# Optimization experiments

Hardware: AMD Instinct MI355X
Metric: run time of the kernel (lower is better)

Reference implementation:

```python
import jax, jax.numpy as jnp
import numpy as np

H = 16        # num_heads
D = 128       # head_dim = hidden_size // num_heads
HID = 2048    # hidden_size
BLOCK = 64    # moba_chunk_size
TOPK = 8      # moba_topk


def setup_inputs() -> dict:
    key = jax.random.key(0)
    ks = jax.random.split(key, 5)
    B, S = 1, 2048
    hidden_states = jax.random.normal(ks[0], (B, S, HID), dtype=jnp.float32)
    scale = HID ** -0.5
    Wq = jax.random.normal(ks[1], (HID, H * D), dtype=jnp.float32) * scale
    Wk = jax.random.normal(ks[2], (HID, H * D), dtype=jnp.float32) * scale
    Wv = jax.random.normal(ks[3], (HID, H * D), dtype=jnp.float32) * scale
    Wo = jax.random.normal(ks[4], (H * D, HID), dtype=jnp.float32) * scale
    return {"hidden_states": hidden_states, "Wq": Wq, "Wk": Wk, "Wv": Wv, "Wo": Wo}


def _moba_forward(hidden_states, Wq, Wk, Wv, Wo):
    B, S, _ = hidden_states.shape
    nb = S // BLOCK
    INF = jnp.float32(jnp.inf)

    q = (hidden_states @ Wq).reshape(B, S, H, D)
    k = (hidden_states @ Wk).reshape(B, S, H, D)
    v = (hidden_states @ Wv).reshape(B, S, H, D)

    # MoBA gating: mean-pooled key per block -> [B, nb, H, D]
    kg = k.reshape(B, nb, BLOCK, H, D).mean(axis=2)
    gate = jnp.einsum('bshd,bnhd->bhsn', q, kg)  # [B,H,S,nb]

    pos = jnp.arange(S)
    qb = pos // BLOCK                 # query's own block
    blk = jnp.arange(nb)
    is_self = qb[:, None] == blk[None, :]                      # self block always selected
    not_past = pos[:, None] < (blk[None, :] + 1) * BLOCK       # blocks not fully in the past
    gate = jnp.where(is_self, INF, jnp.where(not_past, -INF, gate))

    kk = min(TOPK, nb)
    topv, topi = jax.lax.top_k(gate, kk)                       # [B,H,S,kk]
    thresh = topv.min(axis=-1, keepdims=True)
    idx_mask = (topi[..., None] == blk).any(axis=-2)           # [B,H,S,nb]
    need = (gate >= thresh) & idx_mask
    gate_bias = jnp.where(need, 0.0, -INF)                     # additive block mask

    sm_scale = D ** -0.5
    qk = jnp.einsum('bshd,bthd->bhst', q, k) * sm_scale        # [B,H,S,S]
    qk = qk.reshape(B, H, S, nb, BLOCK) + gate_bias[..., None]
    qk = qk.reshape(B, H, S, S)
    causal = pos[:, None] >= pos[None, :]
    qk = jnp.where(causal, qk, -INF)

    p = jax.nn.softmax(qk, axis=-1)
    o = jnp.einsum('bhst,bthd->bshd', p, v).reshape(B, S, H * D)
    return o @ Wo


def reference(hidden_states, Wq, Wk, Wv, Wo):
    # Returns (output, attentions=None, past_key_values=None) in the original;
    # only the output tensor matters for correctness.
    return _moba_forward(hidden_states, Wq, Wk, Wv, Wo)
```

## Files before the change

kernel.cpp:

```cpp
#include <hip/hip_runtime.h>
#include <hip/hip_bf16.h>
#include <stdint.h>
#include <stddef.h>


using bh = __bf16;
typedef __bf16 bhx8 __attribute__((ext_vector_type(8)));
typedef __bf16 bhx4 __attribute__((ext_vector_type(4)));
typedef float  f32x4 __attribute__((ext_vector_type(4)));

#define SEQ   2048
#define HIDN  2048
#define NHEAD 16
#define HDIM  128
#define NBLK  32
#define BLKSZ 64
#define NQKV  6144
#define NGATE 512
#define LDC   136
#define PSTRIDE ((size_t)SEQ * NGATE)

#define GLDS16(gsrc, ldst)                                                     \
  __builtin_amdgcn_global_load_lds(                                            \
      (const __attribute__((address_space(1))) uint32_t*)(gsrc),               \
      (__attribute__((address_space(3))) uint32_t*)(ldst), 16, 0, 0)

__global__ __launch_bounds__(256) void prep(const float* __restrict__ hs,
                                            bh* __restrict__ hs_hi, bh* __restrict__ hs_lo,
                                            const float* __restrict__ Wq, const float* __restrict__ Wk,
                                            const float* __restrict__ Wv, const float* __restrict__ Wo,
                                            bh* __restrict__ wqkvT, bh* __restrict__ woT,
                                            float* __restrict__ hsm) {
  __shared__ float tile[32][33];
  const int b = blockIdx.x;
  const int t = threadIdx.x;
  if (b < 16384) {
    const int z = b >> 12;
    const int x = b & 63, y = (b >> 6) & 63;
    const float* in = (z == 0) ? Wq : (z == 1) ? Wk : (z == 2) ? Wv : Wo;
    bh* out = (z < 3) ? (wqkvT + (size_t)z * HIDN * HIDN) : woT;
    const int tx = t & 31, ty = t >> 5;
    const int c0 = x * 32, r0 = y * 32;
#pragma unroll
    for (int i = 0; i < 4; i++)
      tile[ty + i * 8][tx] = in[(size_t)(r0 + ty + i * 8) * HIDN + c0 + tx];
    __syncthreads();
#pragma unroll
    for (int i = 0; i < 4; i++)
      out[(size_t)(c0 + ty + i * 8) * HIDN + r0 + tx] = (bh)tile[tx][ty + i * 8];
  } else if (b < 16384 + 4096) {
    int i = ((b - 16384) * 256 + t) * 4;
    float4 v = *(const float4*)(hs + i);
    bhx4 h4, l4;
    float vv[4] = {v.x, v.y, v.z, v.w};
#pragma unroll
    for (int e = 0; e < 4; e++) {
      bh h = (bh)vv[e];
      h4[e] = h;
      l4[e] = (bh)(vv[e] - (float)h);
    }
    *(bhx4*)(hs_hi + i) = h4;
    *(bhx4*)(hs_lo + i) = l4;
  } else {
    int idx = (b - 20480) * 256 + t;
    int n = idx >> 11, c = idx & 2047;
    const float* p = hs + (size_t)(n * BLKSZ) * HIDN + c;
    float s = 0.f;
#pragma unroll 8
    for (int r = 0; r < BLKSZ; r++) s += p[(size_t)r * HIDN];
    hsm[idx] = s * (1.0f / 64.0f);
  }
}

#define GEMM_STAGE_TILE(SRC, r0_, ldsbase)                                       \
  {                                                                              \
    _Pragma("unroll")                                                            \
    for (int it_ = 0; it_ < 4; it_++) {                                          \
      int idx_ = it_ * 256 + t;                                                  \
      int row_ = idx_ >> 3, x_ = (idx_ & 7) << 4;                                \
      GLDS16((const char*)(SRC) + (size_t)(r0_ + row_) * strideB + kbyte +       \
                 (x_ ^ ((row_ & 7) << 4)),                                       \
             (char*)(ldsbase) + ((idx_ >> 6) << 10));                            \
    }                                                                            \
  }

__global__ __launch_bounds__(256) void qkvkg(const bh* __restrict__ A, const bh* __restrict__ BT,
                                             bh* __restrict__ Cb,
                                             const float* __restrict__ hsm,
                                             const float* __restrict__ Wk,
                                             float* __restrict__ part) {
  __shared__ __align__(16) char smraw[128 * LDC * 2];
  const int t = threadIdx.x;

  if (blockIdx.x < 768) {
    bh* smem = (bh*)smraw;
    bh* As = smem;
    bh* Bs = smem + 128 * 64;
    const int L = t & 63, w = t >> 6;
    const int wm = w & 1, wn = w >> 1;
    const int quad = L >> 4, lo = L & 15;
    const int m0 = (blockIdx.x / 48) * 128, n0 = (blockIdx.x % 48) * 128;
    const size_t strideB = (size_t)HIDN * 2;

    f32x4 acc[4][4];
#pragma unroll
    for (int i = 0; i < 4; i++)
#pragma unroll
      for (int j = 0; j < 4; j++) acc[i][j] = (f32x4){0.f, 0.f, 0.f, 0.f};

    for (int k0 = 0; k0 < HIDN; k0 += 64) {
      const size_t kbyte = (size_t)k0 * 2;
      GEMM_STAGE_TILE(A, m0, As);
      GEMM_STAGE_TILE(BT, n0, Bs);
      __syncthreads();
#pragma unroll
      for (int ks = 0; ks < 2; ks++) {
        bhx8 af[4], bf_[4];
#pragma unroll
        for (int i = 0; i < 4; i++) {
          const int row = wm * 64 + i * 16 + lo;
          af[i] = *(const bhx8*)((const char*)As + row * 128 +
                                 ((ks * 64 + quad * 16) ^ ((row & 7) << 4)));
        }
#pragma unroll
        for (int j = 0; j < 4; j++) {
          const int row = wn * 64 + j * 16 + lo;
          bf_[j] = *(const bhx8*)((const char*)Bs + row * 128 +
                                  ((ks * 64 + quad * 16) ^ ((row & 7) << 4)));
        }
#pragma unroll
        for (int i = 0; i < 4; i++)
#pragma unroll
          for (int j = 0; j < 4; j++)
            acc[i][j] = __builtin_amdgcn_mfma_f32_16x16x32_bf16(af[i], bf_[j], acc[i][j], 0, 0, 0);
      }
      __syncthreads();
    }

    bh* Cs = smem;
#pragma unroll
    for (int i = 0; i < 4; i++)
#pragma unroll
      for (int j = 0; j < 4; j++)
#pragma unroll
        for (int r = 0; r < 4; r++)
          Cs[(wm * 64 + i * 16 + quad * 4 + r) * LDC + wn * 64 + j * 16 + lo] = (bh)acc[i][j][r];
    __syncthreads();
#pragma unroll
    for (int it = 0; it < 8; it++) {
      int idx = it * 256 + t;
      int row = idx >> 4, cg = idx & 15;
      *(uint4*)(Cb + (size_t)(m0 + row) * NQKV + n0 + cg * 8) = *(const uint4*)&Cs[row * LDC + cg * 8];
    }
  } else {
    float (*hl)[32] = (float (*)[32])smraw;
    const int b2 = blockIdx.x - 768;
    const int c = (b2 & 7) * 256 + t;
    const int ky = b2 >> 3;
    const int k0 = ky * 32;
    for (int i = t; i < 32 * 32; i += 256)
      hl[i >> 5][i & 31] = hsm[(size_t)(i >> 5) * HIDN + k0 + (i & 31)];
    __syncthreads();
    float acc[32];
#pragma unroll
    for (int n = 0; n < 32; n++) acc[n] = 0.f;
#pragma unroll 2
    for (int k4 = 0; k4 < 8; k4++) {
      float w0 = Wk[(size_t)(k0 + k4 * 4 + 0) * HIDN + c];
      float w1 = Wk[(size_t)(k0 + k4 * 4 + 1) * HIDN + c];
      float w2 = Wk[(size_t)(k0 + k4 * 4 + 2) * HIDN + c];
      float w3 = Wk[(size_t)(k0 + k4 * 4 + 3) * HIDN + c];
#pragma unroll
      for (int n = 0; n < 32; n++) {
        float4 hv = *(const float4*)&hl[n][k4 * 4];
        acc[n] += hv.x * w0 + hv.y * w1 + hv.z * w2 + hv.w * w3;
      }
    }
#pragma unroll
    for (int n = 0; n < 32; n++)
      part[((size_t)ky * 32 + n) * HIDN + c] = acc[n];
  }
}

__global__ __launch_bounds__(256) void gemm_bt128f(const bh* __restrict__ A, const bh* __restrict__ BT,
                                                   float* __restrict__ Cf, int M, int N, int K) {
  __shared__ __align__(16) bh smem[2 * 128 * 64];
  bh* As = smem;
  bh* Bs = smem + 128 * 64;
  const int t = threadIdx.x;
  const int L = t & 63, w = t >> 6;
  const int wm = w & 1, wn = w >> 1;
  const int quad = L >> 4, lo = L & 15;
  const int m0 = blockIdx.y * 128, n0 = blockIdx.x * 128;
  const size_t strideB = (size_t)K * 2;

  f32x4 acc[4][4];
#pragma unroll
  for (int i = 0; i < 4; i++)
#pragma unroll
    for (int j = 0; j < 4; j++) acc[i][j] = (f32x4){0.f, 0.f, 0.f, 0.f};

  for (int k0 = 0; k0 < K; k0 += 64) {
    const size_t kbyte = (size_t)k0 * 2;
    GEMM_STAGE_TILE(A, m0, As);
    GEMM_STAGE_TILE(BT, n0, Bs);
    __syncthreads();
#pragma unroll
    for (int ks = 0; ks < 2; ks++) {
      bhx8 af[4], bf_[4];
#pragma unroll
      for (int i = 0; i < 4; i++) {
        const int row = wm * 64 + i * 16 + lo;
        af[i] = *(const bhx8*)((const char*)As + row * 128 +
                               ((ks * 64 + quad * 16) ^ ((row & 7) << 4)));
      }
#pragma unroll
      for (int j = 0; j < 4; j++) {
        const int row = wn * 64 + j * 16 + lo;
        bf_[j] = *(const bhx8*)((const char*)Bs + row * 128 +
                                ((ks * 64 + quad * 16) ^ ((row & 7) << 4)));
      }
#pragma unroll
      for (int i = 0; i < 4; i++)
#pragma unroll
        for (int j = 0; j < 4; j++)
          acc[i][j] = __builtin_amdgcn_mfma_f32_16x16x32_bf16(af[i], bf_[j], acc[i][j], 0, 0, 0);
    }
    __syncthreads();
  }

#pragma unroll
  for (int i = 0; i < 4; i++)
#pragma unroll
    for (int j = 0; j < 4; j++)
#pragma unroll
      for (int r = 0; r < 4; r++) {
        int row = m0 + wm * 64 + i * 16 + quad * 4 + r;
        int col = n0 + wn * 64 + j * 16 + lo;
        Cf[(size_t)row * N + col] = acc[i][j][r];
      }
}

__global__ __launch_bounds__(256) void gemm_gate_split(const bh* __restrict__ hs_hi,
                                                       const bh* __restrict__ hs_lo,
                                                       const bh* __restrict__ wg_hi,
                                                       const bh* __restrict__ wg_lo,
                                                       float* __restrict__ part6,
                                                       float* __restrict__ part2) {
  __shared__ __align__(16) bh smem[2 * 128 * 64];
  bh* As = smem;
  bh* Bs = smem + 128 * 64;
  const int t = threadIdx.x;
  const int L = t & 63, w = t >> 6;
  const int wm = w & 1, wn = w >> 1;
  const int quad = L >> 4, lo = L & 15;
  const int m0 = blockIdx.y * 128, n0 = blockIdx.x * 128;
  const int z = blockIdx.z;
  const size_t strideB = (size_t)HIDN * 2;

  f32x4 acc[4][4];
#pragma unroll
  for (int i = 0; i < 4; i++)
#pragma unroll
    for (int j = 0; j < 4; j++) acc[i][j] = (f32x4){0.f, 0.f, 0.f, 0.f};

  for (int k0 = 0; k0 < 768; k0 += 64) {
    const int vk = z * 768 + k0;
    const int ph = vk >> 11;
    const bh* Ap = (ph == 1) ? hs_lo : hs_hi;
    const bh* Bp = (ph == 2) ? wg_lo : wg_hi;
    const size_t kbyte = (size_t)(vk & 2047) * 2;
    GEMM_STAGE_TILE(Ap, m0, As);
    GEMM_STAGE_TILE(Bp, n0, Bs);
    __syncthreads();
#pragma unroll
    for (int ks = 0; ks < 2; ks++) {
      bhx8 af[4], bf_[4];
#pragma unroll
      for (int i = 0; i < 4; i++) {
        const int row = wm * 64 + i * 16 + lo;
        af[i] = *(const bhx8*)((const char*)As + row * 128 +
                               ((ks * 64 + quad * 16) ^ ((row & 7) << 4)));
      }
#pragma unroll
      for (int j = 0; j < 4; j++) {
        const int row = wn * 64 + j * 16 + lo;
        bf_[j] = *(const bhx8*)((const char*)Bs + row * 128 +
                                ((ks * 64 + quad * 16) ^ ((row & 7) << 4)));
      }
#pragma unroll
      for (int i = 0; i < 4; i++)
#pragma unroll
        for (int j = 0; j < 4; j++)
          acc[i][j] = __builtin_amdgcn_mfma_f32_16x16x32_bf16(af[i], bf_[j], acc[i][j], 0, 0, 0);
    }
    __syncthreads();
  }

  float* outp = (z < 6) ? (part6 + (size_t)z * PSTRIDE) : (part2 + (size_t)(z - 6) * PSTRIDE);
#pragma unroll
  for (int i = 0; i < 4; i++)
#pragma unroll
    for (int j = 0; j < 4; j++)
#pragma unroll
      for (int r = 0; r < 4; r++) {
        int row = m0 + wm * 64 + i * 16 + quad * 4 + r;
        int col = n0 + wn * 64 + j * 16 + lo;
        outp[(size_t)row * NGATE + col] = acc[i][j][r];
      }
}

__global__ __launch_bounds__(256) void kg_reduce64(const float* __restrict__ part, float* __restrict__ kg) {
  int idx = blockIdx.x * 256 + threadIdx.x;
  float s = 0.f;
#pragma unroll
  for (int kc = 0; kc < 64; kc++) s += part[(size_t)kc * 65536 + idx];
  kg[idx] = s;
}

__global__ __launch_bounds__(256) void wgk_vtrans(const float* __restrict__ Wq,
                                                  const float* __restrict__ kg,
                                                  bh* __restrict__ wg_hi, bh* __restrict__ wg_lo,
                                                  const bh* __restrict__ qkv, bh* __restrict__ vt) {
  __shared__ __align__(16) char smraw[49792];
  const int b = blockIdx.x;
  const int t = threadIdx.x;
  if (b < 4096) {
    float (*tile)[33] = (float (*)[33])smraw;
    const int tx = t & 31, ty = t >> 5;
    const int s0 = (b & 63) * 32, d0 = ((b >> 6) & 3) * 32, h = b >> 8;
#pragma unroll
    for (int i = 0; i < 4; i++)
      tile[ty + i * 8][tx] = (float)qkv[(size_t)(s0 + ty + i * 8) * NQKV + 2 * HIDN + h * HDIM + d0 + tx];
    __syncthreads();
#pragma unroll
    for (int i = 0; i < 4; i++)
      vt[((size_t)h * HDIM + d0 + ty + i * 8) * SEQ + s0 + tx] = (bh)tile[tx][ty + i * 8];
  } else {
    float (*wst)[65] = (float (*)[65])smraw;
    float (*kl)[129] = (float (*)[129])(smraw + 33280);
    const int b2 = b - 4096;
    const int h = b2 >> 3;
    const int r0 = (b2 & 7) * 256;
    const int rloc = t & 63, ng = t >> 6;

    for (int i = t; i < 32 * 128; i += 256)
      kl[i >> 7][i & 127] = kg[(size_t)(i >> 7) * HIDN + h * HDIM + (i & 127)];

#pragma unroll
    for (int rt = 0; rt < 4; rt++) {
      __syncthreads();
      for (int i = t; i < 64 * 128; i += 256) {
        int row = i >> 7, col = i & 127;
        wst[col][row] = Wq[(size_t)(r0 + rt * 64 + row) * HIDN + h * HDIM + col];
      }
      __syncthreads();
      float acc8[8];
#pragma unroll
      for (int nn = 0; nn < 8; nn++) acc8[nn] = 0.f;
      for (int d = 0; d < 128; d++) {
        float wv = wst[d][rloc];
#pragma unroll
        for (int nn = 0; nn < 8; nn++)
          acc8[nn] += wv * kl[ng * 8 + nn][d];
      }
#pragma unroll
      for (int nn = 0; nn < 8; nn++) {
        int n = ng * 8 + nn;
        float v = acc8[nn];
        bh hi = (bh)v;
        size_t off = (size_t)(h * 32 + n) * HIDN + r0 + rt * 64 + rloc;
        wg_hi[off] = hi;
        wg_lo[off] = (bh)(v - (float)hi);
      }
    }
  }
}

__global__ __launch_bounds__(256) void gate_topk(const float* __restrict__ part6,
                                                 const float* __restrict__ part2,
                                                 unsigned* __restrict__ bsel) {
  int w = threadIdx.x >> 6, L = threadIdx.x & 63;
  int p = blockIdx.x * 4 + w;
  int h = p >> 11, s = p & 2047;
  int qb = s >> 6;
  int n = L;
  float g = -1e30f;
  if (n == qb) g = 1e30f;
  else if (n < qb) {
    size_t off = (size_t)s * NGATE + h * 32 + n;
    g = part6[off] + part6[off + PSTRIDE] + part6[off + 2 * PSTRIDE] +
        part6[off + 3 * PSTRIDE] + part6[off + 4 * PSTRIDE] + part6[off + 5 * PSTRIDE] +
        part2[off] + part2[off + PSTRIDE];
  }
  int rank = 0;
#pragma unroll
  for (int j = 0; j < 32; j++) {
    float gj = __shfl(g, j, 64);
    if (gj > g || (gj == g && j < n)) rank++;
  }
  bool sel = (n <= qb) && (n < 32) && (rank < 8);
  unsigned long long bm = __ballot(sel);
  if (L == 0) bsel[p] = (unsigned)(bm & 0xffffffffull);
}

__global__ __launch_bounds__(256) void attn(const bh* __restrict__ qkv, const bh* __restrict__ vt,
                                            const unsigned* __restrict__ bsel, bh* __restrict__ obuf) {
  __shared__ __align__(16) bh Ksm[64 * 128];
  __shared__ __align__(16) bh Vsm[128 * 64];
  __shared__ __align__(16) bh PLb[4][16 * 72];
  __shared__ unsigned ublk;
  const int t = threadIdx.x;
  const int w = t >> 6, L = t & 63;
  const int quad = L >> 4, lo = L & 15;
  const int bid = blockIdx.x;
  const int jj = bid >> 3;
  const int h = ((bid & 7) << 1) | (jj & 1);
  const int qb = (jj < 32) ? (31 - (jj >> 1)) : ((jj - 32) >> 1);
  const int s0 = qb * 64 + w * 16;

  unsigned bs[4];
#pragma unroll
  for (int r = 0; r < 4; r++) bs[r] = bsel[h * SEQ + s0 + quad * 4 + r];
  unsigned uni = bs[0] | bs[1] | bs[2] | bs[3];
  uni |= (unsigned)__shfl_xor((int)uni, 16);
  uni |= (unsigned)__shfl_xor((int)uni, 32);
  const unsigned uniw = uni;
  if (t == 0) ublk = 0;
  __syncthreads();
  if (L == 0) atomicOr(&ublk, uni);
  __syncthreads();
  const unsigned un = ublk;

  bhx8 aq[4];
  const bh* qrow = qkv + (size_t)(s0 + lo) * NQKV + h * HDIM;
#pragma unroll
  for (int ks = 0; ks < 4; ks++) aq[ks] = *(const bhx8*)(qrow + ks * 32 + quad * 8);

  f32x4 oacc[8];
#pragma unroll
  for (int j = 0; j < 8; j++) oacc[j] = (f32x4){0.f, 0.f, 0.f, 0.f};
  f32x4 lacc = (f32x4){0.f, 0.f, 0.f, 0.f};
  float mi[4] = {-1e30f, -1e30f, -1e30f, -1e30f};

  bhx8 ones8;
#pragma unroll
  for (int e = 0; e < 8; e++) ones8[e] = (bh)1.0f;

  const float scale = 0.08838834764831845f;

  unsigned rem = un;
  while (rem) {
    const int ncur = (int)__builtin_ctz(rem);
    rem &= rem - 1;

    {
      const char* ksrc = (const char*)(qkv + (size_t)(ncur * BLKSZ) * NQKV + HIDN + h * HDIM);
      const char* vsrc = (const char*)(vt + ((size_t)h * HDIM) * SEQ + ncur * BLKSZ);
#pragma unroll
      for (int it = 0; it < 4; it++) {
        int idx = it * 256 + t;
        int row = idx >> 4, x = (idx & 15) << 4;
        GLDS16(ksrc + (size_t)row * (NQKV * 2) + (x ^ ((row & 7) << 4)),
               (char*)Ksm + ((idx >> 6) << 10));
      }
#pragma unroll
      for (int it = 0; it < 4; it++) {
        int idx = it * 256 + t;
        int row = idx >> 3, x = (idx & 7) << 4;
        GLDS16(vsrc + (size_t)row * (SEQ * 2) + (x ^ ((row & 7) << 4)),
               (char*)Vsm + ((idx >> 6) << 10));
      }
    }
    __syncthreads();

    if ((uniw >> ncur) & 1) {
      const char* Kc = (const char*)Ksm;
      const char* Vc = (const char*)Vsm;
      const bool self = (ncur == qb);

      f32x4 sc[4];
      __builtin_amdgcn_s_setprio(1);
#pragma unroll
      for (int nt = 0; nt < 4; nt++) {
        f32x4 s4 = (f32x4){0.f, 0.f, 0.f, 0.f};
#pragma unroll
        for (int ks = 0; ks < 4; ks++) {
          const int row = nt * 16 + lo;
          bhx8 bk = *(const bhx8*)(Kc + row * 256 + ((ks * 64 + quad * 16) ^ ((row & 7) << 4)));
          s4 = __builtin_amdgcn_mfma_f32_16x16x32_bf16(aq[ks], bk, s4, 0, 0, 0);
        }
        sc[nt] = s4;
      }
      __builtin_amdgcn_s_setprio(0);

      if (self) {
#pragma unroll
        for (int nt = 0; nt < 4; nt++)
#pragma unroll
          for (int r = 0; r < 4; r++) {
            float v = sc[nt][r] * scale;
            int kpos = ncur * BLKSZ + nt * 16 + lo;
            int qpos = s0 + quad * 4 + r;
            bool ok = ((bs[r] >> ncur) & 1) && (kpos <= qpos);
            sc[nt][r] = ok ? v : -1e30f;
          }
      } else {
        float bias[4];
#pragma unroll
        for (int r = 0; r < 4; r++)
          bias[r] = ((bs[r] >> ncur) & 1) ? 0.f : -1e30f;
#pragma unroll
        for (int nt = 0; nt < 4; nt++)
#pragma unroll
          for (int r = 0; r < 4; r++)
            sc[nt][r] = sc[nt][r] * scale + bias[r];
      }
      float rm[4];
#pragma unroll
      for (int r = 0; r < 4; r++)
        rm[r] = fmaxf(fmaxf(sc[0][r], sc[1][r]), fmaxf(sc[2][r], sc[3][r]));
#pragma unroll
      for (int off = 1; off < 16; off <<= 1)
#pragma unroll
        for (int r = 0; r < 4; r++) rm[r] = fmaxf(rm[r], __shfl_xor(rm[r], off));

      bool exceed = (rm[0] > mi[0] + 8.f) || (rm[1] > mi[1] + 8.f) ||
                    (rm[2] > mi[2] + 8.f) || (rm[3] > mi[3] + 8.f);
      if (__any(exceed)) {
        float alpha[4];
#pragma unroll
        for (int r = 0; r < 4; r++) {
          float nm = fmaxf(mi[r], rm[r]);
          alpha[r] = __expf(mi[r] - nm);
          mi[r] = nm;
        }
#pragma unroll
        for (int j = 0; j < 8; j++)
#pragma unroll
          for (int r = 0; r < 4; r++) oacc[j][r] *= alpha[r];
#pragma unroll
        for (int r = 0; r < 4; r++) lacc[r] *= alpha[r];
      }

#pragma unroll
      for (int nt = 0; nt < 4; nt++)
#pragma unroll
        for (int r = 0; r < 4; r++) {
          float pv = __expf(sc[nt][r] - mi[r]);
          PLb[w][(quad * 4 + r) * 72 + nt * 16 + lo] = (bh)pv;
        }

      __builtin_amdgcn_s_setprio(1);
#pragma unroll
      for (int kk = 0; kk < 2; kk++) {
        bhx8 pa = *(const bhx8*)&PLb[w][lo * 72 + kk * 32 + quad * 8];
        lacc = __builtin_amdgcn_mfma_f32_16x16x32_bf16(pa, ones8, lacc, 0, 0, 0);
#pragma unroll
        for (int j = 0; j < 8; j++) {
          const int row = j * 16 + lo;
          bhx8 vv = *(const bhx8*)(Vc + row * 128 + ((kk * 64 + quad * 16) ^ ((row & 7) << 4)));
          oacc[j] = __builtin_amdgcn_mfma_f32_16x16x32_bf16(pa, vv, oacc[j], 0, 0, 0);
        }
      }
      __builtin_amdgcn_s_setprio(0);
    }

    __syncthreads();
  }

#pragma unroll
  for (int j = 0; j < 8; j++)
#pragma unroll
    for (int r = 0; r < 4; r++) {
      int row = s0 + quad * 4 + r;
      int col = h * HDIM + j * 16 + lo;
      obuf[(size_t)row * HIDN + col] = (bh)(oacc[j][r] / lacc[r]);
    }
}

extern "C" void kernel_launch(void* const* d_in, const int* in_sizes, int n_in,
                              void* d_out, int out_size, void* d_ws, size_t ws_size,
                              hipStream_t stream) {
  const float* hs = (const float*)d_in[0];
  const float* Wq = (const float*)d_in[1];
  const float* Wk = (const float*)d_in[2];
  const float* Wv = (const float*)d_in[3];
  const float* Wo = (const float*)d_in[4];

  char* ws = (char*)d_ws;
  bh* hs_hi = (bh*)ws;            ws += (size_t)SEQ * HIDN * 2;
  bh* hs_lo = (bh*)ws;            ws += (size_t)SEQ * HIDN * 2;
  bh* wqkvT = (bh*)ws;            ws += (size_t)NQKV * HIDN * 2;
  bh* woT = (bh*)ws;              ws += (size_t)HIDN * HIDN * 2;
  bh* qkv = (bh*)ws;              ws += (size_t)SEQ * NQKV * 2;
  bh* vt = (bh*)ws;               ws += (size_t)NHEAD * HDIM * SEQ * 2;
  bh* obuf = (bh*)ws;             ws += (size_t)SEQ * HIDN * 2;
  float* hsm = (float*)ws;        ws += (size_t)NBLK * HIDN * 4;
  float* kg = (float*)ws;         ws += (size_t)NBLK * HIDN * 4;
  bh* wg_hi = (bh*)ws;            ws += (size_t)NGATE * HIDN * 2;
  bh* wg_lo = (bh*)ws;            ws += (size_t)NGATE * HIDN * 2;
  unsigned* bsel = (unsigned*)ws; ws += (size_t)NHEAD * SEQ * 4;
  float* kg_part = (float*)vt;
  float* gpart6 = (float*)wqkvT;
  float* gpart2 = (float*)obuf;

  prep<<<16384 + 4096 + 256, 256, 0, stream>>>(hs, hs_hi, hs_lo, Wq, Wk, Wv, Wo, wqkvT, woT, hsm);

  qkvkg<<<768 + 512, 256, 0, stream>>>(hs_hi, wqkvT, qkv, hsm, Wk, kg_part);

  kg_reduce64<<<(NBLK * HIDN) / 256, 256, 0, stream>>>(kg_part, kg);
  wgk_vtrans<<<4096 + 128, 256, 0, stream>>>(Wq, kg, wg_hi, wg_lo, qkv, vt);
  gemm_gate_split<<<dim3(NGATE / 128, SEQ / 128, 8), 256, 0, stream>>>(
      hs_hi, hs_lo, wg_hi, wg_lo, gpart6, gpart2);
  gate_topk<<<(NHEAD * SEQ) / 4, 256, 0, stream>>>(gpart6, gpart2, bsel);

  attn<<<dim3(NBLK * NHEAD), 256, 0, stream>>>(qkv, vt, bsel, obuf);

  gemm_bt128f<<<dim3(HIDN / 128, SEQ / 128), 256, 0, stream>>>(obuf, woT, (float*)d_out, SEQ, HIDN, HIDN);
}
```

Measured before the change: 417.3 us.

## Split long attention query blocks across two workgroups and skip masked gate GEMM tiles

Query blocks 16-31 of attention now run as two workgroups, one over key blocks 0-15 and one over 16..qb. Each writes unnormalized partial outputs plus row max and sum to a scratch buffer, and a new combine kernel merges them with the usual log-sum-exp rescaling. The gate weight layout is reordered to block-major (n*16+h), so the gate GEMM launches only the tiles that hold causally reachable blocks (40 instead of 64 per split). This evens out the triangular attention load and cuts wasted gate work, at the cost of an extra kernel launch and a scratch round-trip through global memory.

```diff
diff --git a/kernel.cpp b/kernel.cpp
--- a/kernel.cpp
+++ b/kernel.cpp
@@ -19,6 +19,7 @@
 #define NGATE 512
 #define LDC   136
 #define PSTRIDE ((size_t)SEQ * NGATE)
+#define POMSTRIDE 8320
 
 #define GLDS16(gsrc, ldst)                                                     \
   __builtin_amdgcn_global_load_lds(                                            \
@@ -254,7 +255,13 @@
   const int L = t & 63, w = t >> 6;
   const int wm = w & 1, wn = w >> 1;
   const int quad = L >> 4, lo = L & 15;
-  const int m0 = blockIdx.y * 128, n0 = blockIdx.x * 128;
+  const int t40 = blockIdx.x;
+  int cc, mm;
+  if (t40 < 16)      { cc = 0; mm = t40; }
+  else if (t40 < 28) { cc = 1; mm = t40 - 12; }
+  else if (t40 < 36) { cc = 2; mm = t40 - 20; }
+  else               { cc = 3; mm = t40 - 24; }
+  const int m0 = mm * 128, n0 = cc * 128;
   const int z = blockIdx.z;
   const size_t strideB = (size_t)HIDN * 2;
 
@@ -369,7 +376,7 @@
         int n = ng * 8 + nn;
         float v = acc8[nn];
         bh hi = (bh)v;
-        size_t off = (size_t)(h * 32 + n) * HIDN + r0 + rt * 64 + rloc;
+        size_t off = (size_t)(n * 16 + h) * HIDN + r0 + rt * 64 + rloc;
         wg_hi[off] = hi;
         wg_lo[off] = (bh)(v - (float)hi);
       }
@@ -388,7 +395,7 @@
   float g = -1e30f;
   if (n == qb) g = 1e30f;
   else if (n < qb) {
-    size_t off = (size_t)s * NGATE + h * 32 + n;
+    size_t off = (size_t)s * NGATE + n * 16 + h;
     g = part6[off] + part6[off + PSTRIDE] + part6[off + 2 * PSTRIDE] +
         part6[off + 3 * PSTRIDE] + part6[off + 4 * PSTRIDE] + part6[off + 5 * PSTRIDE] +
         part2[off] + part2[off + PSTRIDE];
@@ -405,7 +412,8 @@
 }
 
 __global__ __launch_bounds__(256) void attn(const bh* __restrict__ qkv, const bh* __restrict__ vt,
-                                            const unsigned* __restrict__ bsel, bh* __restrict__ obuf) {
+                                            const unsigned* __restrict__ bsel, bh* __restrict__ obuf,
+                                            float* __restrict__ pom) {
   __shared__ __align__(16) bh Ksm[64 * 128];
   __shared__ __align__(16) bh Vsm[128 * 64];
   __shared__ __align__(16) bh PLb[4][16 * 72];
@@ -416,12 +424,21 @@
   const int bid = blockIdx.x;
   const int jj = bid >> 3;
   const int h = ((bid & 7) << 1) | (jj & 1);
-  const int qb = (jj < 32) ? (31 - (jj >> 1)) : ((jj - 32) >> 1);
+  const int il = jj >> 1;
+  const int i16 = il & 15, grp = il >> 4;
+  const int actual = (grp == 0) ? i16 : (grp == 1) ? (31 - i16) : (32 + i16);
+  int qb, nlo, nhi, part;
+  bool split;
+  if (actual < 16)      { qb = actual + 16; part = 1; nlo = 16; nhi = qb; split = true; }
+  else if (actual < 32) { qb = actual - 16; part = 0; nlo = 0;  nhi = qb; split = false; }
+  else                  { qb = actual - 16; part = 0; nlo = 0;  nhi = 15; split = true; }
+  const unsigned wmask = ((nhi == 31) ? 0xFFFFFFFFu : ((1u << (nhi + 1)) - 1)) &
+                         (0xFFFFFFFFu << nlo);
   const int s0 = qb * 64 + w * 16;
 
   unsigned bs[4];
 #pragma unroll
-  for (int r = 0; r < 4; r++) bs[r] = bsel[h * SEQ + s0 + quad * 4 + r];
+  for (int r = 0; r < 4; r++) bs[r] = bsel[h * SEQ + s0 + quad * 4 + r] & wmask;
   unsigned uni = bs[0] | bs[1] | bs[2] | bs[3];
   uni |= (unsigned)__shfl_xor((int)uni, 16);
   uni |= (unsigned)__shfl_xor((int)uni, 32);
@@ -569,14 +586,63 @@
     __syncthreads();
   }
 
-#pragma unroll
-  for (int j = 0; j < 8; j++)
-#pragma unroll
-    for (int r = 0; r < 4; r++) {
-      int row = s0 + quad * 4 + r;
-      int col = h * HDIM + j * 16 + lo;
-      obuf[(size_t)row * HIDN + col] = (bh)(oacc[j][r] / lacc[r]);
-    }
+  if (!split) {
+#pragma unroll
+    for (int j = 0; j < 8; j++)
+#pragma unroll
+      for (int r = 0; r < 4; r++) {
+        int row = s0 + quad * 4 + r;
+        int col = h * HDIM + j * 16 + lo;
+        obuf[(size_t)row * HIDN + col] = (bh)(oacc[j][r] / lacc[r]);
+      }
+  } else {
+    float* slab = pom + (size_t)((h * 16 + (qb - 16)) * 2 + part) * POMSTRIDE;
+    const int rl0 = w * 16 + quad * 4;
+#pragma unroll
+    for (int j = 0; j < 8; j++)
+#pragma unroll
+      for (int r = 0; r < 4; r++)
+        slab[(rl0 + r) * 128 + j * 16 + lo] = oacc[j][r];
+    if (lo == 0) {
+#pragma unroll
+      for (int r = 0; r < 4; r++) {
+        slab[8192 + rl0 + r] = mi[r];
+        slab[8256 + rl0 + r] = lacc[r];
+      }
+    }
+  }
+}
+
+__global__ __launch_bounds__(256) void attn_combine(const float* __restrict__ pom,
+                                                    bh* __restrict__ obuf) {
+  const int b = blockIdx.x;
+  const int h = b >> 4, qs = b & 15;
+  const int t = threadIdx.x;
+  const float* s0 = pom + (size_t)((h * 16 + qs) * 2 + 0) * POMSTRIDE;
+  const float* s1 = s0 + POMSTRIDE;
+  const int rl = t >> 2;
+  const int c0 = (t & 3) * 32;
+  float m0 = s0[8192 + rl], l0 = s0[8256 + rl];
+  float m1 = s1[8192 + rl], l1 = s1[8256 + rl];
+  float m = fmaxf(m0, m1);
+  float a0 = __expf(m0 - m), a1 = __expf(m1 - m);
+  float inv = 1.f / (l0 * a0 + l1 * a1);
+  a0 *= inv; a1 *= inv;
+  const int row = (qs + 16) * 64 + rl;
+  bh* orow = obuf + (size_t)row * HIDN + h * HDIM + c0;
+  const float* p0 = s0 + rl * 128 + c0;
+  const float* p1 = s1 + rl * 128 + c0;
+#pragma unroll
+  for (int c = 0; c < 32; c += 4) {
+    float4 v0 = *(const float4*)(p0 + c);
+    float4 v1 = *(const float4*)(p1 + c);
+    bhx4 o4;
+    o4[0] = (bh)(v0.x * a0 + v1.x * a1);
+    o4[1] = (bh)(v0.y * a0 + v1.y * a1);
+    o4[2] = (bh)(v0.z * a0 + v1.z * a1);
+    o4[3] = (bh)(v0.w * a0 + v1.w * a1);
+    *(bhx4*)(orow + c) = o4;
+  }
 }
 
 extern "C" void kernel_launch(void* const* d_in, const int* in_sizes, int n_in,
@@ -604,6 +670,7 @@
   float* kg_part = (float*)vt;
   float* gpart6 = (float*)wqkvT;
   float* gpart2 = (float*)obuf;
+  float* pom = (float*)wqkvT;
 
   prep<<<16384 + 4096 + 256, 256, 0, stream>>>(hs, hs_hi, hs_lo, Wq, Wk, Wv, Wo, wqkvT, woT, hsm);
 
@@ -611,11 +678,12 @@
 
   kg_reduce64<<<(NBLK * HIDN) / 256, 256, 0, stream>>>(kg_part, kg);
   wgk_vtrans<<<4096 + 128, 256, 0, stream>>>(Wq, kg, wg_hi, wg_lo, qkv, vt);
-  gemm_gate_split<<<dim3(NGATE / 128, SEQ / 128, 8), 256, 0, stream>>>(
+  gemm_gate_split<<<dim3(40, 1, 8), 256, 0, stream>>>(
       hs_hi, hs_lo, wg_hi, wg_lo, gpart6, gpart2);
   gate_topk<<<(NHEAD * SEQ) / 4, 256, 0, stream>>>(gpart6, gpart2, bsel);
 
-  attn<<<dim3(NBLK * NHEAD), 256, 0, stream>>>(qkv, vt, bsel, obuf);
+  attn<<<768, 256, 0, stream>>>(qkv, vt, bsel, obuf, pom);
+  attn_combine<<<256, 256, 0, stream>>>(pom, obuf);
 
   gemm_bt128f<<<dim3(HIDN / 128, SEQ / 128), 256, 0, stream>>>(obuf, woT, (float*)d_out, SEQ, HIDN, HIDN);
 }
```

After: 409.8 us. About the same (-1.8%).
